# Performance work log

Hardware: AMD Instinct MI355X
Metric: run time of the kernel (lower is better)

The kernel has to match this reference:

```python
import jax, jax.numpy as jnp
import numpy as np
from jax import lax

GROUP_SIZE = 40
K = 5
PAD_L = (K - 1) // 2  # 2
PAD_R = (K - 1) - PAD_L  # 2


def setup_inputs() -> dict:
    key = jax.random.key(0)
    k1, k2, k3 = jax.random.split(key, 3)
    B, C, H, W = 128, 64, 56, 56
    x = jax.random.normal(k1, (B, C, H, W), dtype=jnp.float32)
    kernels = jax.random.normal(k2, (GROUP_SIZE, K, K), dtype=jnp.float32)
    g = jax.random.randint(k3, (B,), 0, GROUP_SIZE, dtype=jnp.int64)
    return {"x": x, "kernels": kernels, "g": g, "l": 0, "n": 2}


def reference(x, kernels, g, l, n):
    # x: [B, C, H, W]; kernels: [group_size, K, K]; g: [B] int indices
    # num_layers=0 -> layer_transforms is None, so l=0 path: plain conv2d.
    B = x.shape[0]
    g = g % kernels.shape[0]
    kernel = kernels[g][:, None, :, :]  # gathered per-sample kernel [B, 1, K, K]
    xt = jnp.transpose(x, (1, 0, 2, 3))  # [C, B, H, W]: batch dim -> channels
    for _ in range(n):  # n is a small static Python int
        # circular padding on spatial dims (F.pad mode='circular')
        xp = jnp.pad(xt, ((0, 0), (0, 0), (PAD_L, PAD_R), (PAD_L, PAD_R)), mode="wrap")
        # grouped conv with groups = B (one kernel per sample); torch conv2d is
        # cross-correlation, matching lax.conv_general_dilated (no kernel flip)
        xt = lax.conv_general_dilated(
            xp, kernel,
            window_strides=(1, 1), padding="VALID",
            feature_group_count=B,
            dimension_numbers=("NCHW", "OIHW", "NCHW"),
        )
    out = jnp.transpose(xt, (1, 0, 2, 3)).reshape(x.shape)
    return out
```

## Files before the change

### kernel.cpp

```cpp
#include <hip/hip_runtime.h>

#define NG 40

__global__ void compose_k2(const float* __restrict__ kernels, float* __restrict__ k2) {
    int t = blockIdx.x * 256 + threadIdx.x;
    if (t >= NG * 81) return;
    int gi = t / 81, r = t - gi * 81;
    int a = r / 9, b = r - a * 9;
    const float* k = kernels + gi * 25;
    float s = 0.f;
    for (int i = 0; i < 5; ++i) {
        int p = a - i;
        if (p < 0 || p > 4) continue;
        for (int j = 0; j < 5; ++j) {
            int q = b - j;
            if (q < 0 || q > 4) continue;
            s += k[i * 5 + j] * k[p * 5 + q];
        }
    }
    k2[t] = s;
}

__device__ __forceinline__ void async_copy16(const float* gsrc, float* lds_dst) {
    __builtin_amdgcn_global_load_lds(
        (const __attribute__((address_space(1))) void*)(gsrc),
        (__attribute__((address_space(3))) void*)(lds_dst),
        16, 0, 0);
}

template <bool USE_WS>
__global__ __launch_bounds__(128, 3)
void conv9_main(const float* __restrict__ x, const float* __restrict__ kdata,
                const int* __restrict__ g, float* __restrict__ out) {
    __shared__ float tile[64 * 72];
    __shared__ float k9s[84];

    const int tid = threadIdx.x;
    const int bx  = blockIdx.x;
    const int b   = bx >> 6;

    int gi = g[b] % NG; if (gi < 0) gi += NG;

    const float* xp = x + (size_t)bx * 3136;
    #pragma unroll
    for (int m = 0; m < 9; ++m) {
        int idx = m * 128 + tid;
        int pr  = idx / 18;
        int seg = idx - pr * 18;
        int sr = pr - 4;      if (sr < 0) sr += 56; if (sr >= 56) sr -= 56;
        int sc = seg * 4 - 4; if (sc < 0) sc += 56; if (sc >= 56) sc -= 56;
        async_copy16(xp + sr * 56 + sc, tile + idx * 4);
    }

    float kk[81];
    if (USE_WS) {
        const float* kp = kdata + gi * 81;
        #pragma unroll
        for (int i = 0; i < 81; ++i) kk[i] = kp[i];
    } else {
        if (tid < 81) {
            const float* k = kdata + gi * 25;
            int a = tid / 9, bb = tid - a * 9;
            float s = 0.f;
            for (int i = 0; i < 5; ++i) {
                int p = a - i;
                if (p < 0 || p > 4) continue;
                for (int j = 0; j < 5; ++j) {
                    int q = bb - j;
                    if (q < 0 || q > 4) continue;
                    s += k[i * 5 + j] * k[p * 5 + q];
                }
            }
            k9s[tid] = s;
        }
    }

    __syncthreads();

    if (!USE_WS) {
        #pragma unroll
        for (int i = 0; i < 81; ++i) kk[i] = k9s[i];
    }

    const int pr = tid >> 4;
    const int pc = tid & 15;
    const int q  = 7 * pr;
    const int c  = 4 * pc;

    float acc[7][4] = {};
    const float* trow = tile + q * 72 + c;

    #pragma unroll
    for (int h = 0; h < 15; ++h) {
        float4 A = *(const float4*)(trow + h * 72);
        float4 B = *(const float4*)(trow + h * 72 + 4);
        float4 C = *(const float4*)(trow + h * 72 + 8);
        float w[12] = {A.x, A.y, A.z, A.w, B.x, B.y, B.z, B.w, C.x, C.y, C.z, C.w};
        #pragma unroll
        for (int ro = 0; ro < 7; ++ro) {
            const int v = h - ro;
            if (v < 0 || v > 8) continue;
            #pragma unroll
            for (int j = 0; j < 4; ++j) {
                #pragma unroll
                for (int u = 0; u < 9; ++u)
                    acc[ro][j] += w[j + u] * kk[v * 9 + u];
            }
        }
    }

    if (pc < 14) {
        float* op = out + (size_t)bx * 3136 + q * 56 + c;
        #pragma unroll
        for (int ro = 0; ro < 7; ++ro)
            *(float4*)(op + ro * 56) =
                make_float4(acc[ro][0], acc[ro][1], acc[ro][2], acc[ro][3]);
    }
}

extern "C" void kernel_launch(void* const* d_in, const int* in_sizes, int n_in,
                              void* d_out, int out_size, void* d_ws, size_t ws_size,
                              hipStream_t stream) {
    const float* x    = (const float*)d_in[0];
    const float* kern = (const float*)d_in[1];
    const int*   g    = (const int*)d_in[2];
    float*       out  = (float*)d_out;

    const bool use_ws = ws_size >= (size_t)(NG * 81 * sizeof(float));
    if (use_ws) {
        compose_k2<<<dim3((NG * 81 + 255) / 256), dim3(256), 0, stream>>>(kern, (float*)d_ws);
        conv9_main<true><<<dim3(8192), dim3(128), 0, stream>>>(x, (const float*)d_ws, g, out);
    } else {
        conv9_main<false><<<dim3(8192), dim3(128), 0, stream>>>(x, kern, g, out);
    }
}
```

Before: 216.2 us.

## Read conv input directly from global memory instead of staging in LDS

Drops the async global-to-LDS staging of the padded 64x72 tile. Each thread now loads its 15 rows of three float4s straight from global memory, with circular wrap handled by precomputed column and row indices. This removes LDS use and the block-wide barrier in the workspace path, and raises the launch-bounds occupancy hint from 3 to 4. In exchange, neighbouring threads re-read overlapping halo data through the cache instead of sharing one LDS copy, and registers become tighter.

```diff
diff --git a/kernel.cpp b/kernel.cpp
--- a/kernel.cpp
+++ b/kernel.cpp
@@ -21,43 +21,23 @@
     k2[t] = s;
 }
 
-__device__ __forceinline__ void async_copy16(const float* gsrc, float* lds_dst) {
-    __builtin_amdgcn_global_load_lds(
-        (const __attribute__((address_space(1))) void*)(gsrc),
-        (__attribute__((address_space(3))) void*)(lds_dst),
-        16, 0, 0);
-}
-
 template <bool USE_WS>
-__global__ __launch_bounds__(128, 3)
-void conv9_main(const float* __restrict__ x, const float* __restrict__ kdata,
-                const int* __restrict__ g, float* __restrict__ out) {
-    __shared__ float tile[64 * 72];
-    __shared__ float k9s[84];
-
+__global__ __launch_bounds__(128, 4)
+void conv9_direct(const float* __restrict__ x, const float* __restrict__ kdata,
+                  const int* __restrict__ g, float* __restrict__ out) {
     const int tid = threadIdx.x;
     const int bx  = blockIdx.x;
     const int b   = bx >> 6;
 
     int gi = g[b] % NG; if (gi < 0) gi += NG;
 
-    const float* xp = x + (size_t)bx * 3136;
-    #pragma unroll
-    for (int m = 0; m < 9; ++m) {
-        int idx = m * 128 + tid;
-        int pr  = idx / 18;
-        int seg = idx - pr * 18;
-        int sr = pr - 4;      if (sr < 0) sr += 56; if (sr >= 56) sr -= 56;
-        int sc = seg * 4 - 4; if (sc < 0) sc += 56; if (sc >= 56) sc -= 56;
-        async_copy16(xp + sr * 56 + sc, tile + idx * 4);
-    }
-
     float kk[81];
-    if (USE_WS) {
+    if constexpr (USE_WS) {
         const float* kp = kdata + gi * 81;
         #pragma unroll
         for (int i = 0; i < 81; ++i) kk[i] = kp[i];
     } else {
+        __shared__ float k9s[84];
         if (tid < 81) {
             const float* k = kdata + gi * 25;
             int a = tid / 9, bb = tid - a * 9;
@@ -73,28 +53,32 @@
             }
             k9s[tid] = s;
         }
-    }
-
-    __syncthreads();
-
-    if (!USE_WS) {
+        __syncthreads();
         #pragma unroll
         for (int i = 0; i < 81; ++i) kk[i] = k9s[i];
     }
 
-    const int pr = tid >> 4;
+    const int rg = tid >> 4;
     const int pc = tid & 15;
-    const int q  = 7 * pr;
+    const int q  = 7 * rg;
     const int c  = 4 * pc;
 
+    int c0 = c - 4; if (c0 < 0) c0 += 56; if (c0 >= 56) c0 -= 56;
+    int c1 = c;     if (c1 >= 56) c1 -= 56;
+    int c2 = c + 4; if (c2 >= 56) c2 -= 56;
+
+    const float* xp = x + (size_t)bx * 3136;
+    int r = q - 4; if (r < 0) r += 56;
+
     float acc[7][4] = {};
-    const float* trow = tile + q * 72 + c;
 
     #pragma unroll
     for (int h = 0; h < 15; ++h) {
-        float4 A = *(const float4*)(trow + h * 72);
-        float4 B = *(const float4*)(trow + h * 72 + 4);
-        float4 C = *(const float4*)(trow + h * 72 + 8);
+        const float* rp = xp + r * 56;
+        float4 A = *(const float4*)(rp + c0);
+        float4 B = *(const float4*)(rp + c1);
+        float4 C = *(const float4*)(rp + c2);
+        ++r; if (r == 56) r = 0;
         float w[12] = {A.x, A.y, A.z, A.w, B.x, B.y, B.z, B.w, C.x, C.y, C.z, C.w};
         #pragma unroll
         for (int ro = 0; ro < 7; ++ro) {
@@ -129,8 +113,8 @@
     const bool use_ws = ws_size >= (size_t)(NG * 81 * sizeof(float));
     if (use_ws) {
         compose_k2<<<dim3((NG * 81 + 255) / 256), dim3(256), 0, stream>>>(kern, (float*)d_ws);
-        conv9_main<true><<<dim3(8192), dim3(128), 0, stream>>>(x, (const float*)d_ws, g, out);
+        conv9_direct<true><<<dim3(8192), dim3(128), 0, stream>>>(x, (const float*)d_ws, g, out);
     } else {
-        conv9_main<false><<<dim3(8192), dim3(128), 0, stream>>>(x, kern, g, out);
+        conv9_direct<false><<<dim3(8192), dim3(128), 0, stream>>>(x, kern, g, out);
     }
 }
```

New measurement: 477.6 us. 2.21x slower.
